# Kernel tuning notes

Hardware: AMD Instinct MI355X
Metric: run time of the kernel (lower is better)

The kernel has to match this reference:

```python
import jax, jax.numpy as jnp
import numpy as np

DIM = 128
KS = 7
HEADS = 4
HEAD_DIM = DIM // HEADS


def setup_inputs() -> dict:
    key = jax.random.key(0)
    ks = jax.random.split(key, 10)
    B, H, W, C = 4, 64, 64, DIM
    s = 0.02
    return {
        "x": jax.random.normal(ks[0], (B, H, W, C), jnp.float32),
        "qkv_w": jax.random.normal(ks[1], (C, 3 * C), jnp.float32) * s,
        "qkv_b": jnp.zeros((3 * C,), jnp.float32),
        "proj_w": jax.random.normal(ks[2], (C, C), jnp.float32) * s,
        "proj_b": jnp.zeros((C,), jnp.float32),
        "rpb": jax.random.normal(ks[3], (HEADS, 2 * KS - 1, 2 * KS - 1), jnp.float32) * s,
        "g1_w": jax.random.normal(ks[4], (C, C // 2), jnp.float32) * s,
        "g1_b": jnp.zeros((C // 2,), jnp.float32),
        "g2_w": jax.random.normal(ks[5], (C // 2, 1), jnp.float32) * s,
        "g2_b": jnp.zeros((1,), jnp.float32),
    }


def _neighborhood_attention(x, qkv_w, qkv_b, proj_w, proj_b, rpb):
    B, H, W, C = x.shape
    k = KS
    # qkv projection -> [B,H,W,3,heads,head_dim]
    qkv = (x @ qkv_w + qkv_b).reshape(B, H, W, 3, HEADS, HEAD_DIM)
    q = qkv[..., 0, :, :] * (HEAD_DIM ** -0.5)  # [B,H,W,h,d]
    kk = qkv[..., 1, :, :]
    v = qkv[..., 2, :, :]

    # Clamped sliding-window start indices (NATTEN semantics)
    sh = jnp.clip(jnp.arange(H) - k // 2, 0, H - k)  # [H]
    sw = jnp.clip(jnp.arange(W) - k // 2, 0, W - k)  # [W]
    idx_h = sh[:, None] + jnp.arange(k)[None, :]  # [H,k]
    idx_w = sw[:, None] + jnp.arange(k)[None, :]  # [W,k]

    # Gather neighborhood windows: [B,H,W,k,k,h,d]
    kwin = kk[:, idx_h[:, None, :, None], idx_w[None, :, None, :]]
    vwin = v[:, idx_h[:, None, :, None], idx_w[None, :, None, :]]

    # Relative position bias indices: (neighbor - query) + (k-1)
    bih = idx_h - jnp.arange(H)[:, None] + (k - 1)  # [H,k]
    biw = idx_w - jnp.arange(W)[:, None] + (k - 1)  # [W,k]
    # bias: [h,H,W,k,k] -> [H,W,h,k,k]
    bias = rpb[:, bih[:, None, :, None], biw[None, :, None, :]]
    bias = jnp.transpose(bias, (1, 2, 0, 3, 4))

    # scores: [B,H,W,h,k,k]
    scores = jnp.einsum('bxyhd,bxyklhd->bxyhkl', q, kwin) + bias[None]
    attn = jax.nn.softmax(scores.reshape(B, H, W, HEADS, k * k), axis=-1)
    attn = attn.reshape(B, H, W, HEADS, k, k)
    out = jnp.einsum('bxyhkl,bxyklhd->bxyhd', attn, vwin).reshape(B, H, W, C)
    return out @ proj_w + proj_b


def reference(x, qkv_w, qkv_b, proj_w, proj_b, rpb, g1_w, g1_b, g2_w, g2_b):
    attn_out = _neighborhood_attention(x, qkv_w, qkv_b, proj_w, proj_b, rpb)
    gate = jax.nn.sigmoid(jax.nn.relu(x @ g1_w + g1_b) @ g2_w + g2_b)  # [B,H,W,1]
    return attn_out * gate + x
```

## Files before the change

### kernel.cpp

```cpp
#include <hip/hip_runtime.h>
#include <hip/hip_bf16.h>
#include <math.h>

#define PIXELS 16384
#define C      128
#define KS     7
#define HEADS  4
#define HD     32
#define QSCALE 0.17677669529663687f

typedef __bf16 bf16x8 __attribute__((ext_vector_type(8)));
typedef __bf16 bf16x2 __attribute__((ext_vector_type(2)));
typedef float  f32x4  __attribute__((ext_vector_type(4)));
typedef float  f32x2  __attribute__((ext_vector_type(2)));

__device__ inline unsigned short f2bf(float f) {
    unsigned int u = __builtin_bit_cast(unsigned int, f);
    u += 0x7FFFu + ((u >> 16) & 1u);
    return (unsigned short)(u >> 16);
}
__device__ inline float bflo(unsigned int u) {
    return __builtin_bit_cast(float, u << 16);
}
__device__ inline float bfhi(unsigned int u) {
    return __builtin_bit_cast(float, u & 0xFFFF0000u);
}

__global__ __launch_bounds__(256) void prep_kernel(
    const float* __restrict__ qkv_w, const float* __restrict__ g1_w,
    const float* __restrict__ qkv_b, const float* __restrict__ g1_b,
    const float* __restrict__ proj_w,
    unsigned short* __restrict__ wT, unsigned short* __restrict__ pT,
    float* __restrict__ bias_ext)
{
    const int blk = blockIdx.x, tid = threadIdx.x;
    if (blk < 56) {
        int n = blk * 8 + (tid >> 5);
        int kq = tid & 31;
        float f0, f1, f2, f3;
        if (n < 384) {
            f0 = qkv_w[(kq*4+0)*384 + n]; f1 = qkv_w[(kq*4+1)*384 + n];
            f2 = qkv_w[(kq*4+2)*384 + n]; f3 = qkv_w[(kq*4+3)*384 + n];
        } else {
            int nn = n - 384;
            f0 = g1_w[(kq*4+0)*64 + nn]; f1 = g1_w[(kq*4+1)*64 + nn];
            f2 = g1_w[(kq*4+2)*64 + nn]; f3 = g1_w[(kq*4+3)*64 + nn];
        }
        ushort4 o; o.x = f2bf(f0); o.y = f2bf(f1); o.z = f2bf(f2); o.w = f2bf(f3);
        *(ushort4*)(wT + n*128 + kq*4) = o;
    } else if (blk < 72) {
        int n = (blk - 56) * 8 + (tid >> 5);
        int kq = tid & 31;
        ushort4 o;
        o.x = f2bf(proj_w[(kq*4+0)*128 + n]);
        o.y = f2bf(proj_w[(kq*4+1)*128 + n]);
        o.z = f2bf(proj_w[(kq*4+2)*128 + n]);
        o.w = f2bf(proj_w[(kq*4+3)*128 + n]);
        *(ushort4*)(pT + n*128 + kq*4) = o;
    } else {
        for (int idx = tid; idx < 448; idx += 256)
            bias_ext[idx] = (idx < 384) ? qkv_b[idx] : g1_b[idx - 384];
    }
}

__global__ __launch_bounds__(256) void gemm_qkvh_fused(
    const float* __restrict__ x, const unsigned short* __restrict__ wT,
    const float* __restrict__ bias_ext, const float* __restrict__ g2_w,
    const float* __restrict__ g2_b, unsigned short* __restrict__ qkvb,
    float* __restrict__ gate)
{
    __shared__ __align__(16) unsigned short As[64*128];
    __shared__ __align__(16) unsigned short Bs[64*128];
    __shared__ __align__(16) unsigned short Cs[64*64];
    const int grp = blockIdx.x;
    const int ntBeg = grp ? 4 : 0, ntEnd = grp ? 7 : 4;
    const int m0 = blockIdx.y * 64;
    const int tid = threadIdx.x;

#pragma unroll
    for (int it = 0; it < 4; it++) {
        int idx = tid + it*256, row = idx >> 4, c = idx & 15;
        const float* src = x + (size_t)(m0+row)*128 + c*8;
        float4 a = *(const float4*)src;
        float4 b2 = *(const float4*)(src + 4);
        uint4 v;
        v.x = (unsigned int)f2bf(a.x)  | ((unsigned int)f2bf(a.y)  << 16);
        v.y = (unsigned int)f2bf(a.z)  | ((unsigned int)f2bf(a.w)  << 16);
        v.z = (unsigned int)f2bf(b2.x) | ((unsigned int)f2bf(b2.y) << 16);
        v.w = (unsigned int)f2bf(b2.z) | ((unsigned int)f2bf(b2.w) << 16);
        *(uint4*)(As + row*128 + ((c ^ (row&7)) << 3)) = v;
    }

    const int wave = tid >> 6, lane = tid & 63;
    const int l15 = lane & 15, quad = lane >> 4;
    const int wm = (wave & 1) * 32, wn = (wave >> 1) * 32;

    for (int nt = ntBeg; nt < ntEnd; nt++) {
        const int n0 = nt * 64;
#pragma unroll
        for (int it = 0; it < 4; it++) {
            int idx = tid + it*256, row = idx >> 4, c = idx & 15;
            uint4 v = *(const uint4*)(wT + (size_t)(n0+row)*128 + c*8);
            *(uint4*)(Bs + row*128 + ((c ^ (row&7)) << 3)) = v;
        }
        __syncthreads();

        f32x4 acc[2][2] = {};
#pragma unroll
        for (int ks = 0; ks < 4; ks++) {
            bf16x8 af[2], bq[2];
#pragma unroll
            for (int mt = 0; mt < 2; mt++) {
                int m = wm + mt*16 + l15;
                af[mt] = *(const bf16x8*)(As + m*128 + (((ks*4+quad) ^ (m&7)) << 3));
            }
#pragma unroll
            for (int ntl = 0; ntl < 2; ntl++) {
                int n = wn + ntl*16 + l15;
                bq[ntl] = *(const bf16x8*)(Bs + n*128 + (((ks*4+quad) ^ (n&7)) << 3));
            }
#pragma unroll
            for (int mt = 0; mt < 2; mt++)
#pragma unroll
                for (int ntl = 0; ntl < 2; ntl++)
                    acc[mt][ntl] = __builtin_amdgcn_mfma_f32_16x16x32_bf16(
                        af[mt], bq[ntl], acc[mt][ntl], 0, 0, 0);
        }

        if (nt < 6) {
#pragma unroll
            for (int ntl = 0; ntl < 2; ntl++) {
                int nl = wn + ntl*16 + l15;
                int ng = n0 + nl;
                float qs = (ng < 128) ? QSCALE : 1.0f;
                float bv = bias_ext[ng];
#pragma unroll
                for (int mt = 0; mt < 2; mt++)
#pragma unroll
                    for (int r = 0; r < 4; r++) {
                        int ml = wm + mt*16 + quad*4 + r;
                        Cs[ml*64 + nl] = f2bf((acc[mt][ntl][r] + bv) * qs);
                    }
            }
            __syncthreads();
            int row = tid >> 2, part = tid & 3;
            uint4 a = *(const uint4*)(Cs + row*64 + part*16);
            uint4 b = *(const uint4*)(Cs + row*64 + part*16 + 8);
            unsigned short* dst = qkvb + (size_t)(m0+row)*384 + n0 + part*16;
            *(uint4*)dst = a;
            *(uint4*)(dst + 8) = b;
        } else {
            float* gpart = (float*)Cs;
            float rs[2][4];
#pragma unroll
            for (int mt = 0; mt < 2; mt++)
#pragma unroll
                for (int r = 0; r < 4; r++) rs[mt][r] = 0.0f;
#pragma unroll
            for (int ntl = 0; ntl < 2; ntl++) {
                int nl = wn + ntl*16 + l15;
                float bv = bias_ext[384 + nl];
                float gw = g2_w[nl];
#pragma unroll
                for (int mt = 0; mt < 2; mt++)
#pragma unroll
                    for (int r = 0; r < 4; r++) {
                        float h = acc[mt][ntl][r] + bv;
                        rs[mt][r] += fmaxf(h, 0.0f) * gw;
                    }
            }
#pragma unroll
            for (int off = 1; off <= 8; off <<= 1)
#pragma unroll
                for (int mt = 0; mt < 2; mt++)
#pragma unroll
                    for (int r = 0; r < 4; r++)
                        rs[mt][r] += __shfl_xor(rs[mt][r], off);
            if (l15 == 0) {
#pragma unroll
                for (int mt = 0; mt < 2; mt++)
#pragma unroll
                    for (int r = 0; r < 4; r++)
                        gpart[(wave >> 1)*64 + wm + mt*16 + quad*4 + r] = rs[mt][r];
            }
            __syncthreads();
            if (tid < 64) {
                float g = gpart[tid] + gpart[64 + tid] + g2_b[0];
                gate[m0 + tid] = 1.0f / (1.0f + __expf(-g));
            }
        }
    }
}

__global__ __launch_bounds__(128) void attn_kernel(
    const unsigned short* __restrict__ qkvb, const float* __restrict__ rpb,
    unsigned short* __restrict__ attnb)
{
    __shared__ __align__(16) unsigned short kvs[196 * 136];
    __shared__ float rpb_lds[2 * 169];

    const int blk = blockIdx.x;
    const int pr = blk & 1;
    const int tile = (blk >> 1) & 63;
    const int b = blk >> 7;
    const int ti0 = (tile >> 3) * 8, tj0 = (tile & 7) * 8;
    int wr0 = ti0 - 3; if (wr0 < 0) wr0 = 0;
    int wc0 = tj0 - 3; if (wc0 < 0) wc0 = 0;

    const int tid = threadIdx.x;
    const int hh = tid >> 6, lane = tid & 63;
    const int h = pr * 2 + hh;
    const int pi = lane >> 3, pj = lane & 7;
    const int i = ti0 + pi, j = tj0 + pj;
    int sh = i - 3; sh = sh < 0 ? 0 : (sh > 57 ? 57 : sh);
    int sw = j - 3; sw = sw < 0 ? 0 : (sw > 57 ? 57 : sw);
    const int dr = sh - wr0, dc = sw - wc0;
    const size_t gp = (size_t)(((b << 6) + i) << 6) + j;

    unsigned int qu[16];
    const unsigned short* qptr = qkvb + gp * 384 + h * 32;
    *(uint4*)(qu + 0)  = *(const uint4*)(qptr + 0);
    *(uint4*)(qu + 4)  = *(const uint4*)(qptr + 8);
    *(uint4*)(qu + 8)  = *(const uint4*)(qptr + 16);
    *(uint4*)(qu + 12) = *(const uint4*)(qptr + 24);

    float rpb_v[3];
#pragma unroll
    for (int t = 0; t < 3; t++) {
        int idx = tid + t * 128;
        rpb_v[t] = (idx < 338) ? rpb[pr * 338 + idx] : 0.0f;
    }

    for (int idx = tid; idx < 196 * 16; idx += 128) {
        int pos = idx >> 4, t = idx & 15;
        int wr = pos / 14, wc = pos - wr * 14;
        int gr = wr0 + wr; if (gr > 63) gr = 63;
        int gc = wc0 + wc; if (gc > 63) gc = 63;
        size_t gpos = (size_t)(((b << 6) + gr) << 6) + gc;
        int src = 128 + ((t >> 3) << 7) + pr * 64 + ((t & 7) << 3);
        uint4 v = *(const uint4*)(qkvb + gpos * 384 + src);
        *(uint4*)(kvs + pos * 136 + ((t >> 3) << 6) + ((t & 7) << 3)) = v;
    }
#pragma unroll
    for (int t = 0; t < 3; t++) {
        int idx = tid + t * 128;
        if (idx < 338) rpb_lds[idx] = rpb_v[t];
    }
    __syncthreads();

    f32x2 acc2[16];
#pragma unroll
    for (int p = 0; p < 16; p++) acc2[p] = (f32x2){0.f, 0.f};
    float ssum = 0.0f;

    const float* rl = rpb_lds + hh * 169;
    const int rbase = (sh - i + 6) * 13 + (sw - j + 6);
    const int hwbase = (dr * 14 + dc) * 136 + hh * 32;

    for (int kr = 0; kr < 7; kr++) {
        const unsigned short* rowp = kvs + hwbase + kr * (14 * 136);
        const int ri = rbase + kr * 13;

        unsigned int ku[16], vu[16];
        *(uint4*)(ku + 0)  = *(const uint4*)(rowp + 0);
        *(uint4*)(ku + 4)  = *(const uint4*)(rowp + 8);
        *(uint4*)(ku + 8)  = *(const uint4*)(rowp + 16);
        *(uint4*)(ku + 12) = *(const uint4*)(rowp + 24);
        *(uint4*)(vu + 0)  = *(const uint4*)(rowp + 64);
        *(uint4*)(vu + 4)  = *(const uint4*)(rowp + 72);
        *(uint4*)(vu + 8)  = *(const uint4*)(rowp + 80);
        *(uint4*)(vu + 12) = *(const uint4*)(rowp + 88);

#pragma unroll
        for (int kc = 0; kc < 7; kc++) {
            unsigned int ku2[16], vu2[16];
            if (kc < 6) {
                const unsigned short* kpn = rowp + (kc + 1) * 136;
                *(uint4*)(ku2 + 0)  = *(const uint4*)(kpn + 0);
                *(uint4*)(ku2 + 4)  = *(const uint4*)(kpn + 8);
                *(uint4*)(ku2 + 8)  = *(const uint4*)(kpn + 16);
                *(uint4*)(ku2 + 12) = *(const uint4*)(kpn + 24);
                *(uint4*)(vu2 + 0)  = *(const uint4*)(kpn + 64);
                *(uint4*)(vu2 + 4)  = *(const uint4*)(kpn + 72);
                *(uint4*)(vu2 + 8)  = *(const uint4*)(kpn + 80);
                *(uint4*)(vu2 + 12) = *(const uint4*)(kpn + 88);
            }

            float s0 = rl[ri + kc], s1 = 0.0f, s2 = 0.0f, s3 = 0.0f;
#if __has_builtin(__builtin_amdgcn_fdot2_f32_bf16)
#pragma unroll
            for (int p = 0; p < 4; p++) {
                s0 = __builtin_amdgcn_fdot2_f32_bf16(
                        __builtin_bit_cast(bf16x2, qu[p]),
                        __builtin_bit_cast(bf16x2, ku[p]), s0, false);
                s1 = __builtin_amdgcn_fdot2_f32_bf16(
                        __builtin_bit_cast(bf16x2, qu[p+4]),
                        __builtin_bit_cast(bf16x2, ku[p+4]), s1, false);
                s2 = __builtin_amdgcn_fdot2_f32_bf16(
                        __builtin_bit_cast(bf16x2, qu[p+8]),
                        __builtin_bit_cast(bf16x2, ku[p+8]), s2, false);
                s3 = __builtin_amdgcn_fdot2_f32_bf16(
                        __builtin_bit_cast(bf16x2, qu[p+12]),
                        __builtin_bit_cast(bf16x2, ku[p+12]), s3, false);
            }
#else
#pragma unroll
            for (int p = 0; p < 4; p++) {
                s0 += bflo(qu[p])    * bflo(ku[p])    + bfhi(qu[p])    * bfhi(ku[p]);
                s1 += bflo(qu[p+4])  * bflo(ku[p+4])  + bfhi(qu[p+4])  * bfhi(ku[p+4]);
                s2 += bflo(qu[p+8])  * bflo(ku[p+8])  + bfhi(qu[p+8])  * bfhi(ku[p+8]);
                s3 += bflo(qu[p+12]) * bflo(ku[p+12]) + bfhi(qu[p+12]) * bfhi(ku[p+12]);
            }
#endif
            float e = __expf((s0 + s1) + (s2 + s3));
            ssum += e;

            f32x2 e2 = {e, e};
#pragma unroll
            for (int p = 0; p < 16; p++) {
                f32x2 v2 = {bflo(vu[p]), bfhi(vu[p])};
                acc2[p] += e2 * v2;
            }

            if (kc < 6) {
#pragma unroll
                for (int p = 0; p < 16; p++) { ku[p] = ku2[p]; vu[p] = vu2[p]; }
            }
        }
    }

    const float inv = 1.0f / ssum;
    unsigned int o[16];
#pragma unroll
    for (int p = 0; p < 16; p++) {
        unsigned int lo = f2bf(acc2[p].x * inv);
        unsigned int hi = f2bf(acc2[p].y * inv);
        o[p] = lo | (hi << 16);
    }
    unsigned short* op = attnb + gp * 128 + h * 32;
    *(uint4*)(op + 0)  = *(const uint4*)(o + 0);
    *(uint4*)(op + 8)  = *(const uint4*)(o + 4);
    *(uint4*)(op + 16) = *(const uint4*)(o + 8);
    *(uint4*)(op + 24) = *(const uint4*)(o + 12);
}

__global__ __launch_bounds__(256) void gemm_proj_mfma(
    const unsigned short* __restrict__ ab, const unsigned short* __restrict__ pT,
    const float* __restrict__ proj_b, const float* __restrict__ gate,
    const float* __restrict__ x, float* __restrict__ out)
{
    __shared__ __align__(16) unsigned short As[64*128];
    __shared__ __align__(16) unsigned short Bs[64*128];
    const int n0 = blockIdx.x * 64;
    const int m0 = blockIdx.y * 64;
    const int tid = threadIdx.x;

#pragma unroll
    for (int it = 0; it < 4; it++) {
        int idx = tid + it*256, row = idx >> 4, c = idx & 15;
        uint4 v = *(const uint4*)(ab + (size_t)(m0+row)*128 + c*8);
        *(uint4*)(As + row*128 + ((c ^ (row&7)) << 3)) = v;
    }
#pragma unroll
    for (int it = 0; it < 4; it++) {
        int idx = tid + it*256, row = idx >> 4, c = idx & 15;
        uint4 v = *(const uint4*)(pT + (size_t)(n0+row)*128 + c*8);
        *(uint4*)(Bs + row*128 + ((c ^ (row&7)) << 3)) = v;
    }
    __syncthreads();

    const int wave = tid >> 6, lane = tid & 63;
    const int l15 = lane & 15, quad = lane >> 4;
    const int wm = (wave & 1) * 32, wn = (wave >> 1) * 32;

    f32x4 acc[2][2] = {};
#pragma unroll
    for (int ks = 0; ks < 4; ks++) {
        bf16x8 af[2], bq[2];
#pragma unroll
        for (int mt = 0; mt < 2; mt++) {
            int m = wm + mt*16 + l15;
            af[mt] = *(const bf16x8*)(As + m*128 + (((ks*4+quad) ^ (m&7)) << 3));
        }
#pragma unroll
        for (int ntl = 0; ntl < 2; ntl++) {
            int n = wn + ntl*16 + l15;
            bq[ntl] = *(const bf16x8*)(Bs + n*128 + (((ks*4+quad) ^ (n&7)) << 3));
        }
#pragma unroll
        for (int mt = 0; mt < 2; mt++)
#pragma unroll
            for (int ntl = 0; ntl < 2; ntl++)
                acc[mt][ntl] = __builtin_amdgcn_mfma_f32_16x16x32_bf16(
                    af[mt], bq[ntl], acc[mt][ntl], 0, 0, 0);
    }
    __syncthreads();

    float* Cs = (float*)As;
#pragma unroll
    for (int ntl = 0; ntl < 2; ntl++) {
        int nl = wn + ntl*16 + l15;
        float bv = proj_b[n0 + nl];
#pragma unroll
        for (int mt = 0; mt < 2; mt++)
#pragma unroll
            for (int r = 0; r < 4; r++) {
                int ml = wm + mt*16 + quad*4 + r;
                Cs[ml*64 + nl] = acc[mt][ntl][r] + bv;
            }
    }
    __syncthreads();
    int row = tid >> 2, part = tid & 3;
    float gv = gate[m0 + row];
    const float* xr = x + (size_t)(m0+row)*128 + n0 + part*16;
    float* orow = out + (size_t)(m0+row)*128 + n0 + part*16;
#pragma unroll
    for (int q = 0; q < 4; q++) {
        float4 cv = *(const float4*)(Cs + row*64 + part*16 + q*4);
        float4 xv = *(const float4*)(xr + q*4);
        float4 o;
        o.x = cv.x * gv + xv.x; o.y = cv.y * gv + xv.y;
        o.z = cv.z * gv + xv.z; o.w = cv.w * gv + xv.w;
        *(float4*)(orow + q*4) = o;
    }
}

extern "C" void kernel_launch(void* const* d_in, const int* in_sizes, int n_in,
                              void* d_out, int out_size, void* d_ws, size_t ws_size,
                              hipStream_t stream)
{
    const float* x      = (const float*)d_in[0];
    const float* qkv_w  = (const float*)d_in[1];
    const float* qkv_b  = (const float*)d_in[2];
    const float* proj_w = (const float*)d_in[3];
    const float* proj_b = (const float*)d_in[4];
    const float* rpb    = (const float*)d_in[5];
    const float* g1_w   = (const float*)d_in[6];
    const float* g1_b   = (const float*)d_in[7];
    const float* g2_w   = (const float*)d_in[8];
    const float* g2_b   = (const float*)d_in[9];
    float* out = (float*)d_out;

    float* ws        = (float*)d_ws;
    float* gate      = ws;
    float* bias_ext  = gate + 16384;
    unsigned short* wT    = (unsigned short*)(bias_ext + 448);
    unsigned short* pT    = wT + 57344;
    unsigned short* qkvb  = pT + 16384;
    unsigned short* attnb = qkvb + 6291456;

    (void)in_sizes; (void)n_in; (void)out_size; (void)ws_size;

    prep_kernel<<<73, 256, 0, stream>>>(qkv_w, g1_w, qkv_b, g1_b, proj_w,
                                        wT, pT, bias_ext);
    gemm_qkvh_fused<<<dim3(2, 256), 256, 0, stream>>>(x, wT, bias_ext,
                                                      g2_w, g2_b, qkvb, gate);
    attn_kernel<<<512, 128, 0, stream>>>(qkvb, rpb, attnb);
    gemm_proj_mfma<<<dim3(2, 256), 256, 0, stream>>>(attnb, pT, proj_b, gate, x, out);
}
```

Before: 115.9 us.

## Split attention head dim across two lanes, halve tile rows, double grid

The attention kernel now gives each pixel-head to two lanes, each handling 16 of the 32 head dims. Partial QK dot products are combined with a cross-lane shuffle, and tiles shrink from 8x8 to 4x8 pixels, so the grid grows from 512 to 1024 blocks. The goal is more parallelism and fewer registers per thread for better occupancy and latency hiding. The cost is more halo reload per pixel (140 window positions for 32 pixels instead of 196 for 64) and one shuffle per neighbor. The window start is now clamped so the 10x14 window always stays in bounds.

```diff
diff --git a/kernel.cpp b/kernel.cpp
--- a/kernel.cpp
+++ b/kernel.cpp
@@ -196,33 +196,33 @@
     const unsigned short* __restrict__ qkvb, const float* __restrict__ rpb,
     unsigned short* __restrict__ attnb)
 {
-    __shared__ __align__(16) unsigned short kvs[196 * 136];
+    __shared__ __align__(16) unsigned short kvs[140 * 136];
     __shared__ float rpb_lds[2 * 169];
 
     const int blk = blockIdx.x;
     const int pr = blk & 1;
-    const int tile = (blk >> 1) & 63;
-    const int b = blk >> 7;
-    const int ti0 = (tile >> 3) * 8, tj0 = (tile & 7) * 8;
-    int wr0 = ti0 - 3; if (wr0 < 0) wr0 = 0;
-    int wc0 = tj0 - 3; if (wc0 < 0) wc0 = 0;
+    const int tile = (blk >> 1) & 127;
+    const int b = blk >> 8;
+    const int ti0 = (tile >> 3) * 4, tj0 = (tile & 7) * 8;
+    int wr0 = ti0 - 3; wr0 = wr0 < 0 ? 0 : (wr0 > 54 ? 54 : wr0);
+    int wc0 = tj0 - 3; wc0 = wc0 < 0 ? 0 : (wc0 > 50 ? 50 : wc0);
 
     const int tid = threadIdx.x;
     const int hh = tid >> 6, lane = tid & 63;
     const int h = pr * 2 + hh;
-    const int pi = lane >> 3, pj = lane & 7;
+    const int half = lane >> 5;
+    const int p5 = lane & 31;
+    const int pi = p5 >> 3, pj = p5 & 7;
     const int i = ti0 + pi, j = tj0 + pj;
     int sh = i - 3; sh = sh < 0 ? 0 : (sh > 57 ? 57 : sh);
     int sw = j - 3; sw = sw < 0 ? 0 : (sw > 57 ? 57 : sw);
     const int dr = sh - wr0, dc = sw - wc0;
     const size_t gp = (size_t)(((b << 6) + i) << 6) + j;
 
-    unsigned int qu[16];
-    const unsigned short* qptr = qkvb + gp * 384 + h * 32;
-    *(uint4*)(qu + 0)  = *(const uint4*)(qptr + 0);
-    *(uint4*)(qu + 4)  = *(const uint4*)(qptr + 8);
-    *(uint4*)(qu + 8)  = *(const uint4*)(qptr + 16);
-    *(uint4*)(qu + 12) = *(const uint4*)(qptr + 24);
+    unsigned int qu[8];
+    const unsigned short* qptr = qkvb + gp * 384 + h * 32 + half * 16;
+    *(uint4*)(qu + 0) = *(const uint4*)(qptr + 0);
+    *(uint4*)(qu + 4) = *(const uint4*)(qptr + 8);
 
     float rpb_v[3];
 #pragma unroll
@@ -231,12 +231,10 @@
         rpb_v[t] = (idx < 338) ? rpb[pr * 338 + idx] : 0.0f;
     }
 
-    for (int idx = tid; idx < 196 * 16; idx += 128) {
+    for (int idx = tid; idx < 140 * 16; idx += 128) {
         int pos = idx >> 4, t = idx & 15;
         int wr = pos / 14, wc = pos - wr * 14;
-        int gr = wr0 + wr; if (gr > 63) gr = 63;
-        int gc = wc0 + wc; if (gc > 63) gc = 63;
-        size_t gpos = (size_t)(((b << 6) + gr) << 6) + gc;
+        size_t gpos = (size_t)(((b << 6) + (wr0 + wr)) << 6) + (wc0 + wc);
         int src = 128 + ((t >> 3) << 7) + pr * 64 + ((t & 7) << 3);
         uint4 v = *(const uint4*)(qkvb + gpos * 384 + src);
         *(uint4*)(kvs + pos * 136 + ((t >> 3) << 6) + ((t & 7) << 3)) = v;
@@ -248,45 +246,37 @@
     }
     __syncthreads();
 
-    f32x2 acc2[16];
-#pragma unroll
-    for (int p = 0; p < 16; p++) acc2[p] = (f32x2){0.f, 0.f};
+    f32x2 acc2[8];
+#pragma unroll
+    for (int p = 0; p < 8; p++) acc2[p] = (f32x2){0.f, 0.f};
     float ssum = 0.0f;
 
     const float* rl = rpb_lds + hh * 169;
     const int rbase = (sh - i + 6) * 13 + (sw - j + 6);
-    const int hwbase = (dr * 14 + dc) * 136 + hh * 32;
+    const int hwbase = (dr * 14 + dc) * 136 + hh * 32 + half * 16;
 
     for (int kr = 0; kr < 7; kr++) {
         const unsigned short* rowp = kvs + hwbase + kr * (14 * 136);
         const int ri = rbase + kr * 13;
 
-        unsigned int ku[16], vu[16];
-        *(uint4*)(ku + 0)  = *(const uint4*)(rowp + 0);
-        *(uint4*)(ku + 4)  = *(const uint4*)(rowp + 8);
-        *(uint4*)(ku + 8)  = *(const uint4*)(rowp + 16);
-        *(uint4*)(ku + 12) = *(const uint4*)(rowp + 24);
-        *(uint4*)(vu + 0)  = *(const uint4*)(rowp + 64);
-        *(uint4*)(vu + 4)  = *(const uint4*)(rowp + 72);
-        *(uint4*)(vu + 8)  = *(const uint4*)(rowp + 80);
-        *(uint4*)(vu + 12) = *(const uint4*)(rowp + 88);
+        unsigned int ku[8], vu[8];
+        *(uint4*)(ku + 0) = *(const uint4*)(rowp + 0);
+        *(uint4*)(ku + 4) = *(const uint4*)(rowp + 8);
+        *(uint4*)(vu + 0) = *(const uint4*)(rowp + 64);
+        *(uint4*)(vu + 4) = *(const uint4*)(rowp + 72);
 
 #pragma unroll
         for (int kc = 0; kc < 7; kc++) {
-            unsigned int ku2[16], vu2[16];
+            unsigned int ku2[8], vu2[8];
             if (kc < 6) {
                 const unsigned short* kpn = rowp + (kc + 1) * 136;
-                *(uint4*)(ku2 + 0)  = *(const uint4*)(kpn + 0);
-                *(uint4*)(ku2 + 4)  = *(const uint4*)(kpn + 8);
-                *(uint4*)(ku2 + 8)  = *(const uint4*)(kpn + 16);
-                *(uint4*)(ku2 + 12) = *(const uint4*)(kpn + 24);
-                *(uint4*)(vu2 + 0)  = *(const uint4*)(kpn + 64);
-                *(uint4*)(vu2 + 4)  = *(const uint4*)(kpn + 72);
-                *(uint4*)(vu2 + 8)  = *(const uint4*)(kpn + 80);
-                *(uint4*)(vu2 + 12) = *(const uint4*)(kpn + 88);
-            }
-
-            float s0 = rl[ri + kc], s1 = 0.0f, s2 = 0.0f, s3 = 0.0f;
+                *(uint4*)(ku2 + 0) = *(const uint4*)(kpn + 0);
+                *(uint4*)(ku2 + 4) = *(const uint4*)(kpn + 8);
+                *(uint4*)(vu2 + 0) = *(const uint4*)(kpn + 64);
+                *(uint4*)(vu2 + 4) = *(const uint4*)(kpn + 72);
+            }
+
+            float s0 = 0.0f, s1 = 0.0f;
 #if __has_builtin(__builtin_amdgcn_fdot2_f32_bf16)
 #pragma unroll
             for (int p = 0; p < 4; p++) {
@@ -296,52 +286,44 @@
                 s1 = __builtin_amdgcn_fdot2_f32_bf16(
                         __builtin_bit_cast(bf16x2, qu[p+4]),
                         __builtin_bit_cast(bf16x2, ku[p+4]), s1, false);
-                s2 = __builtin_amdgcn_fdot2_f32_bf16(
-                        __builtin_bit_cast(bf16x2, qu[p+8]),
-                        __builtin_bit_cast(bf16x2, ku[p+8]), s2, false);
-                s3 = __builtin_amdgcn_fdot2_f32_bf16(
-                        __builtin_bit_cast(bf16x2, qu[p+12]),
-                        __builtin_bit_cast(bf16x2, ku[p+12]), s3, false);
             }
 #else
 #pragma unroll
             for (int p = 0; p < 4; p++) {
-                s0 += bflo(qu[p])    * bflo(ku[p])    + bfhi(qu[p])    * bfhi(ku[p]);
-                s1 += bflo(qu[p+4])  * bflo(ku[p+4])  + bfhi(qu[p+4])  * bfhi(ku[p+4]);
-                s2 += bflo(qu[p+8])  * bflo(ku[p+8])  + bfhi(qu[p+8])  * bfhi(ku[p+8]);
-                s3 += bflo(qu[p+12]) * bflo(ku[p+12]) + bfhi(qu[p+12]) * bfhi(ku[p+12]);
+                s0 += bflo(qu[p])   * bflo(ku[p])   + bfhi(qu[p])   * bfhi(ku[p]);
+                s1 += bflo(qu[p+4]) * bflo(ku[p+4]) + bfhi(qu[p+4]) * bfhi(ku[p+4]);
             }
 #endif
-            float e = __expf((s0 + s1) + (s2 + s3));
+            float s = s0 + s1;
+            s += __shfl_xor(s, 32);
+            float e = __expf(s + rl[ri + kc]);
             ssum += e;
 
             f32x2 e2 = {e, e};
 #pragma unroll
-            for (int p = 0; p < 16; p++) {
+            for (int p = 0; p < 8; p++) {
                 f32x2 v2 = {bflo(vu[p]), bfhi(vu[p])};
                 acc2[p] += e2 * v2;
             }
 
             if (kc < 6) {
 #pragma unroll
-                for (int p = 0; p < 16; p++) { ku[p] = ku2[p]; vu[p] = vu2[p]; }
+                for (int p = 0; p < 8; p++) { ku[p] = ku2[p]; vu[p] = vu2[p]; }
             }
         }
     }
 
     const float inv = 1.0f / ssum;
-    unsigned int o[16];
-#pragma unroll
-    for (int p = 0; p < 16; p++) {
+    unsigned int o[8];
+#pragma unroll
+    for (int p = 0; p < 8; p++) {
         unsigned int lo = f2bf(acc2[p].x * inv);
         unsigned int hi = f2bf(acc2[p].y * inv);
         o[p] = lo | (hi << 16);
     }
-    unsigned short* op = attnb + gp * 128 + h * 32;
-    *(uint4*)(op + 0)  = *(const uint4*)(o + 0);
-    *(uint4*)(op + 8)  = *(const uint4*)(o + 4);
-    *(uint4*)(op + 16) = *(const uint4*)(o + 8);
-    *(uint4*)(op + 24) = *(const uint4*)(o + 12);
+    unsigned short* op = attnb + gp * 128 + h * 32 + half * 16;
+    *(uint4*)(op + 0) = *(const uint4*)(o + 0);
+    *(uint4*)(op + 8) = *(const uint4*)(o + 4);
 }
 
 __global__ __launch_bounds__(256) void gemm_proj_mfma(
@@ -455,6 +437,6 @@
                                         wT, pT, bias_ext);
     gemm_qkvh_fused<<<dim3(2, 256), 256, 0, stream>>>(x, wT, bias_ext,
                                                       g2_w, g2_b, qkvb, gate);
-    attn_kernel<<<512, 128, 0, stream>>>(qkvb, rpb, attnb);
+    attn_kernel<<<1024, 128, 0, stream>>>(qkvb, rpb, attnb);
     gemm_proj_mfma<<<dim3(2, 256), 256, 0, stream>>>(attnb, pT, proj_b, gate, x, out);
 }
```

Result: no change. 115.8 us (-0.1%).
